# Performance work log

Hardware: AMD Instinct MI355X
Metric: run time of the kernel (lower is better)

The kernel has to match this reference:

```python
import jax, jax.numpy as jnp
import numpy as np

B, T, D, HD = 4, 4096, 1024, 64

def setup_inputs() -> dict:
    key = jax.random.key(0)
    k1, k2, k3, k4 = jax.random.split(key, 4)
    scale = 1.0 / np.sqrt(D)
    return {
        "x": jax.random.normal(k1, (B, T, D), dtype=jnp.float32),
        "Wq": jax.random.normal(k2, (HD, D), dtype=jnp.float32) * scale,
        "Wk": jax.random.normal(k3, (HD, D), dtype=jnp.float32) * scale,
        "Wv": jax.random.normal(k4, (HD, D), dtype=jnp.float32) * scale,
    }

def reference(x, Wq, Wk, Wv):
    # x: [B,T,D]; W*: [head_dim, D] (torch Linear weight layout)
    Q = jnp.einsum('btd,hd->bth', x, Wq)  # [B,T,HD]
    K = jnp.einsum('btd,hd->bth', x, Wk)
    V = jnp.einsum('btd,hd->bth', x, Wv)
    hd = Q.shape[-1]
    scores = jnp.einsum('bqh,bkh->bqk', Q, K) * (hd ** -0.5)  # [B,T,T]
    t = scores.shape[1]
    causal = jnp.tril(jnp.ones((t, t), dtype=bool))
    scores = jnp.where(causal, scores, -jnp.inf)
    att = jax.nn.softmax(scores, axis=-1)
    return jnp.einsum('bqk,bkh->bqh', att, V)  # [B,T,HD]
```

## Files before the change

kernel.cpp:

```cpp
#include <hip/hip_runtime.h>
#include <stdint.h>

#define B_  4
#define T_  4096
#define D_  1024
#define HD_ 64
#define BT_ 16384

typedef short bf16x8 __attribute__((ext_vector_type(8)));
typedef float f32x4  __attribute__((ext_vector_type(4)));
typedef unsigned short u16;
typedef u16 u16x4 __attribute__((ext_vector_type(4)));

#define M0_ 8.0f

__device__ __forceinline__ u16 f2bf(float f) {
    union { float f; unsigned u; } v; v.f = f;
    unsigned r = (v.u + 0x7FFF + ((v.u >> 16) & 1)) >> 16;
    return (u16)r;
}
__device__ __forceinline__ float bf2f(u16 u) {
    union { unsigned u; float f; } v; v.u = ((unsigned)u) << 16;
    return v.f;
}

__device__ __forceinline__ int slot_base(int qt) {
    int a = qt >> 3, r = qt & 7;
    return (a + 1) * (4 * a + r);
}

__global__ __launch_bounds__(256) void wconv_kernel(
    const float* __restrict__ wq, const float* __restrict__ wk,
    const float* __restrict__ wv, u16* __restrict__ wb)
{
    const int j   = blockIdx.x >> 5;
    const int off = (blockIdx.x & 31) * 2048 + threadIdx.x * 8;
    const float* src = (j == 0) ? wq : ((j == 1) ? wk : wv);
    f32x4 a0 = *(const f32x4*)(src + off);
    f32x4 a1 = *(const f32x4*)(src + off + 4);
    bf16x8 b;
    #pragma unroll
    for (int i = 0; i < 4; ++i) { b[i] = (short)f2bf(a0[i]); b[4 + i] = (short)f2bf(a1[i]); }
    *(bf16x8*)(wb + j * 65536 + off) = b;
}

__global__ __launch_bounds__(256) void qkv_kernel(
    const float* __restrict__ x, const u16* __restrict__ wb,
    u16* __restrict__ qs, u16* __restrict__ kss, u16* __restrict__ vssT)
{
    __shared__ __align__(16) u16 xt[16][72];
    __shared__ __align__(16) u16 wt[192][72];

    const int tid  = threadIdx.x;
    const int lane = tid & 63;
    const int w    = tid >> 6;
    const int quad = lane >> 4;
    const int l16  = lane & 15;
    const int row0 = blockIdx.x * 16;

    const int xrow = tid >> 4;
    const int xcg  = tid & 15;

    f32x4 acc[3];
    #pragma unroll
    for (int g = 0; g < 3; ++g) acc[g] = (f32x4)0.0f;

    f32x4  xr;
    bf16x8 wr[6];
    {
        xr = *(const f32x4*)(x + (size_t)(row0 + xrow) * D_ + xcg * 4);
        #pragma unroll
        for (int i = 0; i < 6; ++i) {
            int chunk = tid + 256 * i;
            wr[i] = *(const bf16x8*)(wb + (size_t)(chunk >> 3) * D_ + (chunk & 7) * 8);
        }
    }

    for (int kc = 0; kc < 16; ++kc) {
        __syncthreads();
        {
            u16x4 px;
            #pragma unroll
            for (int i = 0; i < 4; ++i) px[i] = f2bf(xr[i]);
            *(u16x4*)&xt[xrow][xcg * 4] = px;
            #pragma unroll
            for (int i = 0; i < 6; ++i) {
                int chunk = tid + 256 * i;
                *(bf16x8*)&wt[chunk >> 3][(chunk & 7) * 8] = wr[i];
            }
        }
        __syncthreads();
        if (kc < 15) {
            xr = *(const f32x4*)(x + (size_t)(row0 + xrow) * D_ + (kc + 1) * 64 + xcg * 4);
            #pragma unroll
            for (int i = 0; i < 6; ++i) {
                int chunk = tid + 256 * i;
                wr[i] = *(const bf16x8*)(wb + (size_t)(chunk >> 3) * D_ + (kc + 1) * 64 + (chunk & 7) * 8);
            }
        }
        #pragma unroll
        for (int ks = 0; ks < 2; ++ks) {
            bf16x8 a = *(const bf16x8*)&xt[l16][ks * 32 + quad * 8];
            #pragma unroll
            for (int g = 0; g < 3; ++g) {
                bf16x8 b = *(const bf16x8*)&wt[(w * 3 + g) * 16 + l16][ks * 32 + quad * 8];
                acc[g] = __builtin_amdgcn_mfma_f32_16x16x32_bf16(a, b, acc[g], 0, 0, 0);
            }
        }
    }
    #pragma unroll
    for (int g = 0; g < 3; ++g) {
        const int n = (w * 3 + g) * 16 + l16;
        const int j = n >> 6, h = n & 63;
        const int rbase = row0 + quad * 4;
        if (j == 0) {
            #pragma unroll
            for (int r = 0; r < 4; ++r) qs[(size_t)(rbase + r) * HD_ + h] = f2bf(acc[g][r] * 0.125f);
        } else if (j == 1) {
            #pragma unroll
            for (int r = 0; r < 4; ++r) kss[(size_t)(rbase + r) * HD_ + h] = f2bf(acc[g][r]);
        } else {
            u16x4 v;
            #pragma unroll
            for (int r = 0; r < 4; ++r) v[r] = f2bf(acc[g][r]);
            *(u16x4*)(vssT + (size_t)h * BT_ + rbase) = v;
        }
    }
}

__global__ __launch_bounds__(256) void attn_kernel(
    const u16* __restrict__ qs, const u16* __restrict__ kss,
    const u16* __restrict__ vssT,
    float* __restrict__ pl, u16* __restrict__ pO)
{
    __shared__ __align__(16) u16 kt[64][72];
    __shared__ __align__(16) u16 vt[80][72];
    __shared__ __align__(16) u16 pt[4][16][72];

    const int bi = blockIdx.x;
    const int c  = bi & 7;
    const int qt = (bi >> 3) & 63;
    const int b  = bi >> 9;
    const int kt0 = c * 8;
    if (kt0 > qt) return;
    const int kend = ((kt0 + 7) < qt) ? (kt0 + 7) : qt;

    const int tid  = threadIdx.x;
    const int lane = tid & 63;
    const int w    = tid >> 6;
    const int quad = lane >> 4;
    const int l16  = lane & 15;
    const int qb   = qt * 64;
    const size_t base = (size_t)b * T_;

    for (int idx = tid; idx < 16 * 72; idx += 256) {
        int rr = idx / 72, cc = idx - rr * 72;
        vt[64 + rr][cc] = (rr == 0) ? (u16)0x3F80 : (u16)0;
    }

    bf16x8 qf[2];
    {
        const u16* qp = qs + (base + qb + w * 16 + l16) * HD_ + quad * 8;
        qf[0] = *(const bf16x8*)(qp);
        qf[1] = *(const bf16x8*)(qp + 32);
    }

    f32x4 o_acc[5];
    #pragma unroll
    for (int g = 0; g < 5; ++g) o_acc[g] = (f32x4)0.0f;

    const int lr = tid >> 2, lp = tid & 3;

    bf16x8 kr0, kr1, vr0, vr1;
    {
        const u16* sk = kss + (base + kt0 * 64 + lr) * HD_ + lp * 16;
        kr0 = *(const bf16x8*)(sk);  kr1 = *(const bf16x8*)(sk + 8);
        const u16* sv = vssT + (size_t)lr * BT_ + base + kt0 * 64 + lp * 16;
        vr0 = *(const bf16x8*)(sv);  vr1 = *(const bf16x8*)(sv + 8);
    }

    for (int kti = kt0; kti <= kend; ++kti) {
        __syncthreads();
        *(bf16x8*)&kt[lr][lp * 16]     = kr0;
        *(bf16x8*)&kt[lr][lp * 16 + 8] = kr1;
        *(bf16x8*)&vt[lr][lp * 16]     = vr0;
        *(bf16x8*)&vt[lr][lp * 16 + 8] = vr1;
        __syncthreads();
        if (kti < kend) {
            const u16* sk = kss + (base + (kti + 1) * 64 + lr) * HD_ + lp * 16;
            kr0 = *(const bf16x8*)(sk);  kr1 = *(const bf16x8*)(sk + 8);
            const u16* sv = vssT + (size_t)lr * BT_ + base + (kti + 1) * 64 + lp * 16;
            vr0 = *(const bf16x8*)(sv);  vr1 = *(const bf16x8*)(sv + 8);
        }

        f32x4 s[4];
        #pragma unroll
        for (int g = 0; g < 4; ++g) {
            s[g] = (f32x4)0.0f;
            #pragma unroll
            for (int ks = 0; ks < 2; ++ks) {
                bf16x8 kf = *(const bf16x8*)&kt[g * 16 + l16][ks * 32 + quad * 8];
                s[g] = __builtin_amdgcn_mfma_f32_16x16x32_bf16(qf[ks], kf, s[g], 0, 0, 0);
            }
        }
        if (kti == qt) {
            #pragma unroll
            for (int g = 0; g < 4; ++g) {
                int key = kti * 64 + g * 16 + l16;
                #pragma unroll
                for (int r = 0; r < 4; ++r) {
                    int q = qb + w * 16 + quad * 4 + r;
                    if (key > q) s[g][r] = -1e30f;
                }
            }
        }
        #pragma unroll
        for (int g = 0; g < 4; ++g)
            #pragma unroll
            for (int r = 0; r < 4; ++r)
                pt[w][quad * 4 + r][g * 16 + l16] = f2bf(__expf(s[g][r] - M0_));
        #pragma unroll
        for (int ks = 0; ks < 2; ++ks) {
            bf16x8 pa = *(const bf16x8*)&pt[w][l16][ks * 32 + quad * 8];
            #pragma unroll
            for (int g = 0; g < 5; ++g) {
                bf16x8 vf = *(const bf16x8*)&vt[g * 16 + l16][ks * 32 + quad * 8];
                o_acc[g] = __builtin_amdgcn_mfma_f32_16x16x32_bf16(pa, vf, o_acc[g], 0, 0, 0);
            }
        }
    }

    const int slot = b * 288 + slot_base(qt) + c;
    if (l16 == 0) {
        #pragma unroll
        for (int r = 0; r < 4; ++r)
            pl[slot * 64 + w * 16 + quad * 4 + r] = o_acc[4][r];
    }
    #pragma unroll
    for (int g = 0; g < 4; ++g) {
        #pragma unroll
        for (int r = 0; r < 4; ++r) {
            int row = w * 16 + quad * 4 + r;
            pO[(size_t)slot * 4096 + row * 64 + g * 16 + l16] = f2bf(o_acc[g][r]);
        }
    }
}

__global__ __launch_bounds__(256) void merge_kernel(
    const float* __restrict__ pl, const u16* __restrict__ pO,
    float* __restrict__ out)
{
    const int bi = blockIdx.x;
    const int qt = bi & 63, b = bi >> 6;
    const int nc = (qt >> 3) + 1;
    const int s0 = b * 288 + slot_base(qt);
    const int row = threadIdx.x >> 2;
    const int hg  = (threadIdx.x & 3) * 16;

    float L = 0.0f;
    for (int c2 = 0; c2 < nc; ++c2) L += pl[(s0 + c2) * 64 + row];

    float o[16];
    #pragma unroll
    for (int i = 0; i < 16; ++i) o[i] = 0.0f;
    for (int c2 = 0; c2 < nc; ++c2) {
        const u16* p = pO + (size_t)(s0 + c2) * 4096 + row * 64 + hg;
        bf16x8 v0 = *(const bf16x8*)p;
        bf16x8 v1 = *(const bf16x8*)(p + 8);
        #pragma unroll
        for (int i = 0; i < 8; ++i) {
            o[i]     += bf2f((u16)v0[i]);
            o[8 + i] += bf2f((u16)v1[i]);
        }
    }
    const float inv = 1.0f / L;
    float* op = out + ((size_t)b * T_ + qt * 64 + row) * HD_ + hg;
    #pragma unroll
    for (int j = 0; j < 4; ++j) {
        f32x4 v;
        #pragma unroll
        for (int i = 0; i < 4; ++i) v[i] = o[j * 4 + i] * inv;
        *(f32x4*)(op + j * 4) = v;
    }
}

extern "C" void kernel_launch(void* const* d_in, const int* in_sizes, int n_in,
                              void* d_out, int out_size, void* d_ws, size_t ws_size,
                              hipStream_t stream) {
    const float* x  = (const float*)d_in[0];
    const float* wq = (const float*)d_in[1];
    const float* wk = (const float*)d_in[2];
    const float* wv = (const float*)d_in[3];

    const size_t NE = (size_t)BT_ * HD_;
    char* ws = (char*)d_ws;
    u16* qs   = (u16*)ws;
    u16* kss  = qs  + NE;
    u16* vssT = kss + NE;
    u16* wb   = vssT + NE;
    float* pl = (float*)(wb + 192 * 1024);
    u16* pO   = (u16*)(pl + 1152 * 64);
    float* out = (float*)d_out;

    wconv_kernel<<<dim3(96),   dim3(256), 0, stream>>>(wq, wk, wv, wb);
    qkv_kernel  <<<dim3(1024), dim3(256), 0, stream>>>(x, wb, qs, kss, vssT);
    attn_kernel <<<dim3(2048), dim3(256), 0, stream>>>(qs, kss, vssT, pl, pO);
    merge_kernel<<<dim3(256),  dim3(256), 0, stream>>>(pl, pO, out);
}
```

Before: 167.9 us.

## Drop LDS staging for K/V and weights, give each wave its own query strip

```diff
diff --git a/kernel.cpp b/kernel.cpp
--- a/kernel.cpp
+++ b/kernel.cpp
@@ -22,11 +22,6 @@
 __device__ __forceinline__ float bf2f(u16 u) {
     union { unsigned u; float f; } v; v.u = ((unsigned)u) << 16;
     return v.f;
-}
-
-__device__ __forceinline__ int slot_base(int qt) {
-    int a = qt >> 3, r = qt & 7;
-    return (a + 1) * (4 * a + r);
 }
 
 __global__ __launch_bounds__(256) void wconv_kernel(
@@ -44,12 +39,11 @@
     *(bf16x8*)(wb + j * 65536 + off) = b;
 }
 
-__global__ __launch_bounds__(256) void qkv_kernel(
+__global__ __launch_bounds__(256, 5) void qkv_kernel(
     const float* __restrict__ x, const u16* __restrict__ wb,
     u16* __restrict__ qs, u16* __restrict__ kss, u16* __restrict__ vssT)
 {
-    __shared__ __align__(16) u16 xt[16][72];
-    __shared__ __align__(16) u16 wt[192][72];
+    __shared__ __align__(16) u16 xt[2][16][72];
 
     const int tid  = threadIdx.x;
     const int lane = tid & 63;
@@ -61,52 +55,61 @@
     const int xrow = tid >> 4;
     const int xcg  = tid & 15;
 
+    size_t wrow[3];
+    #pragma unroll
+    for (int g = 0; g < 3; ++g) wrow[g] = (size_t)((w * 3 + g) * 16 + l16) * D_;
+
     f32x4 acc[3];
     #pragma unroll
     for (int g = 0; g < 3; ++g) acc[g] = (f32x4)0.0f;
 
-    f32x4  xr;
-    bf16x8 wr[6];
+    const float* xbase = x + (size_t)(row0 + xrow) * D_ + xcg * 4;
+
+    f32x4 xr = *(const f32x4*)(xbase);
     {
-        xr = *(const f32x4*)(x + (size_t)(row0 + xrow) * D_ + xcg * 4);
-        #pragma unroll
-        for (int i = 0; i < 6; ++i) {
-            int chunk = tid + 256 * i;
-            wr[i] = *(const bf16x8*)(wb + (size_t)(chunk >> 3) * D_ + (chunk & 7) * 8);
-        }
-    }
+        u16x4 px;
+        #pragma unroll
+        for (int i = 0; i < 4; ++i) px[i] = f2bf(xr[i]);
+        *(u16x4*)&xt[0][xrow][xcg * 4] = px;
+    }
+    xr = *(const f32x4*)(xbase + 64);
+
+    bf16x8 wcur[6], wnxt[6];
+    #pragma unroll
+    for (int g = 0; g < 3; ++g)
+        #pragma unroll
+        for (int ks = 0; ks < 2; ++ks)
+            wcur[g * 2 + ks] = *(const bf16x8*)(wb + wrow[g] + ks * 32 + quad * 8);
+
+    __syncthreads();
 
     for (int kc = 0; kc < 16; ++kc) {
+        const int p = kc & 1;
+        if (kc + 1 < 16) {
+            u16x4 px;
+            #pragma unroll
+            for (int i = 0; i < 4; ++i) px[i] = f2bf(xr[i]);
+            *(u16x4*)&xt[p ^ 1][xrow][xcg * 4] = px;
+        }
+        if (kc + 2 < 16)
+            xr = *(const f32x4*)(xbase + (kc + 2) * 64);
+        if (kc + 1 < 16) {
+            #pragma unroll
+            for (int g = 0; g < 3; ++g)
+                #pragma unroll
+                for (int ks = 0; ks < 2; ++ks)
+                    wnxt[g * 2 + ks] = *(const bf16x8*)(wb + wrow[g] + (kc + 1) * 64 + ks * 32 + quad * 8);
+        }
+        bf16x8 a0 = *(const bf16x8*)&xt[p][l16][quad * 8];
+        bf16x8 a1 = *(const bf16x8*)&xt[p][l16][32 + quad * 8];
+        #pragma unroll
+        for (int g = 0; g < 3; ++g) {
+            acc[g] = __builtin_amdgcn_mfma_f32_16x16x32_bf16(a0, wcur[g * 2 + 0], acc[g], 0, 0, 0);
+            acc[g] = __builtin_amdgcn_mfma_f32_16x16x32_bf16(a1, wcur[g * 2 + 1], acc[g], 0, 0, 0);
+        }
+        #pragma unroll
+        for (int i = 0; i < 6; ++i) wcur[i] = wnxt[i];
         __syncthreads();
-        {
-            u16x4 px;
-            #pragma unroll
-            for (int i = 0; i < 4; ++i) px[i] = f2bf(xr[i]);
-            *(u16x4*)&xt[xrow][xcg * 4] = px;
-            #pragma unroll
-            for (int i = 0; i < 6; ++i) {
-                int chunk = tid + 256 * i;
-                *(bf16x8*)&wt[chunk >> 3][(chunk & 7) * 8] = wr[i];
-            }
-        }
-        __syncthreads();
-        if (kc < 15) {
-            xr = *(const f32x4*)(x + (size_t)(row0 + xrow) * D_ + (kc + 1) * 64 + xcg * 4);
-            #pragma unroll
-            for (int i = 0; i < 6; ++i) {
-                int chunk = tid + 256 * i;
-                wr[i] = *(const bf16x8*)(wb + (size_t)(chunk >> 3) * D_ + (kc + 1) * 64 + (chunk & 7) * 8);
-            }
-        }
-        #pragma unroll
-        for (int ks = 0; ks < 2; ++ks) {
-            bf16x8 a = *(const bf16x8*)&xt[l16][ks * 32 + quad * 8];
-            #pragma unroll
-            for (int g = 0; g < 3; ++g) {
-                bf16x8 b = *(const bf16x8*)&wt[(w * 3 + g) * 16 + l16][ks * 32 + quad * 8];
-                acc[g] = __builtin_amdgcn_mfma_f32_16x16x32_bf16(a, b, acc[g], 0, 0, 0);
-            }
-        }
     }
     #pragma unroll
     for (int g = 0; g < 3; ++g) {
@@ -128,89 +131,69 @@
     }
 }
 
-__global__ __launch_bounds__(256) void attn_kernel(
+__global__ __launch_bounds__(256, 4) void attn_kernel(
     const u16* __restrict__ qs, const u16* __restrict__ kss,
     const u16* __restrict__ vssT,
     float* __restrict__ pl, u16* __restrict__ pO)
 {
-    __shared__ __align__(16) u16 kt[64][72];
-    __shared__ __align__(16) u16 vt[80][72];
     __shared__ __align__(16) u16 pt[4][16][72];
-
-    const int bi = blockIdx.x;
-    const int c  = bi & 7;
-    const int qt = (bi >> 3) & 63;
-    const int b  = bi >> 9;
-    const int kt0 = c * 8;
-    if (kt0 > qt) return;
-    const int kend = ((kt0 + 7) < qt) ? (kt0 + 7) : qt;
 
     const int tid  = threadIdx.x;
     const int lane = tid & 63;
     const int w    = tid >> 6;
     const int quad = lane >> 4;
     const int l16  = lane & 15;
-    const int qb   = qt * 64;
+
+    const int j   = blockIdx.x * 4 + w;
+    const int b   = j >> 10;
+    const int rem = j & 1023;
+    const int s   = rem >> 2;
+    const int c   = rem & 3;
+    const int dt  = s >> 2;
+    const int kt0 = c * 16;
+    if (kt0 > dt) return;
+    const int kend = (kt0 + 15 < dt) ? (kt0 + 15) : dt;
+
     const size_t base = (size_t)b * T_;
-
-    for (int idx = tid; idx < 16 * 72; idx += 256) {
-        int rr = idx / 72, cc = idx - rr * 72;
-        vt[64 + rr][cc] = (rr == 0) ? (u16)0x3F80 : (u16)0;
-    }
 
     bf16x8 qf[2];
     {
-        const u16* qp = qs + (base + qb + w * 16 + l16) * HD_ + quad * 8;
+        const u16* qp = qs + (base + s * 16 + l16) * HD_ + quad * 8;
         qf[0] = *(const bf16x8*)(qp);
         qf[1] = *(const bf16x8*)(qp + 32);
     }
+    bf16x8 onesf;
+    {
+        u16 ov = (l16 == 0) ? (u16)0x3F80 : (u16)0;
+        #pragma unroll
+        for (int i = 0; i < 8; ++i) onesf[i] = (short)ov;
+    }
 
     f32x4 o_acc[5];
     #pragma unroll
     for (int g = 0; g < 5; ++g) o_acc[g] = (f32x4)0.0f;
 
-    const int lr = tid >> 2, lp = tid & 3;
-
-    bf16x8 kr0, kr1, vr0, vr1;
-    {
-        const u16* sk = kss + (base + kt0 * 64 + lr) * HD_ + lp * 16;
-        kr0 = *(const bf16x8*)(sk);  kr1 = *(const bf16x8*)(sk + 8);
-        const u16* sv = vssT + (size_t)lr * BT_ + base + kt0 * 64 + lp * 16;
-        vr0 = *(const bf16x8*)(sv);  vr1 = *(const bf16x8*)(sv + 8);
-    }
-
     for (int kti = kt0; kti <= kend; ++kti) {
-        __syncthreads();
-        *(bf16x8*)&kt[lr][lp * 16]     = kr0;
-        *(bf16x8*)&kt[lr][lp * 16 + 8] = kr1;
-        *(bf16x8*)&vt[lr][lp * 16]     = vr0;
-        *(bf16x8*)&vt[lr][lp * 16 + 8] = vr1;
-        __syncthreads();
-        if (kti < kend) {
-            const u16* sk = kss + (base + (kti + 1) * 64 + lr) * HD_ + lp * 16;
-            kr0 = *(const bf16x8*)(sk);  kr1 = *(const bf16x8*)(sk + 8);
-            const u16* sv = vssT + (size_t)lr * BT_ + base + (kti + 1) * 64 + lp * 16;
-            vr0 = *(const bf16x8*)(sv);  vr1 = *(const bf16x8*)(sv + 8);
-        }
-
-        f32x4 s[4];
+        const int kb = kti * 64;
+        f32x4 sv[4];
         #pragma unroll
         for (int g = 0; g < 4; ++g) {
-            s[g] = (f32x4)0.0f;
+            sv[g] = (f32x4)0.0f;
             #pragma unroll
             for (int ks = 0; ks < 2; ++ks) {
-                bf16x8 kf = *(const bf16x8*)&kt[g * 16 + l16][ks * 32 + quad * 8];
-                s[g] = __builtin_amdgcn_mfma_f32_16x16x32_bf16(qf[ks], kf, s[g], 0, 0, 0);
+                bf16x8 kf = *(const bf16x8*)(kss + (base + kb + g * 16 + l16) * HD_ + ks * 32 + quad * 8);
+                sv[g] = __builtin_amdgcn_mfma_f32_16x16x32_bf16(qf[ks], kf, sv[g], 0, 0, 0);
             }
         }
-        if (kti == qt) {
+        if (kti == dt) {
             #pragma unroll
             for (int g = 0; g < 4; ++g) {
-                int key = kti * 64 + g * 16 + l16;
+                int key = kb + g * 16 + l16;
                 #pragma unroll
                 for (int r = 0; r < 4; ++r) {
-                    int q = qb + w * 16 + quad * 4 + r;
-                    if (key > q) s[g][r] = -1e30f;
+                    int q = s * 16 + quad * 4 + r;
+                    if (key > q + 0 * 64) { }
+                    if (key > s * 16 + quad * 4 + r) sv[g][r] = -1e30f;
                 }
             }
         }
@@ -218,31 +201,29 @@
         for (int g = 0; g < 4; ++g)
             #pragma unroll
             for (int r = 0; r < 4; ++r)
-                pt[w][quad * 4 + r][g * 16 + l16] = f2bf(__expf(s[g][r] - M0_));
+                pt[w][quad * 4 + r][g * 16 + l16] = f2bf(__expf(sv[g][r] - M0_));
         #pragma unroll
         for (int ks = 0; ks < 2; ++ks) {
             bf16x8 pa = *(const bf16x8*)&pt[w][l16][ks * 32 + quad * 8];
             #pragma unroll
-            for (int g = 0; g < 5; ++g) {
-                bf16x8 vf = *(const bf16x8*)&vt[g * 16 + l16][ks * 32 + quad * 8];
+            for (int g = 0; g < 4; ++g) {
+                bf16x8 vf = *(const bf16x8*)(vssT + (size_t)(g * 16 + l16) * BT_ + base + kb + ks * 32 + quad * 8);
                 o_acc[g] = __builtin_amdgcn_mfma_f32_16x16x32_bf16(pa, vf, o_acc[g], 0, 0, 0);
             }
-        }
-    }
-
-    const int slot = b * 288 + slot_base(qt) + c;
+            o_acc[4] = __builtin_amdgcn_mfma_f32_16x16x32_bf16(pa, onesf, o_acc[4], 0, 0, 0);
+        }
+    }
+
     if (l16 == 0) {
         #pragma unroll
         for (int r = 0; r < 4; ++r)
-            pl[slot * 64 + w * 16 + quad * 4 + r] = o_acc[4][r];
+            pl[j * 16 + quad * 4 + r] = o_acc[4][r];
     }
     #pragma unroll
     for (int g = 0; g < 4; ++g) {
         #pragma unroll
-        for (int r = 0; r < 4; ++r) {
-            int row = w * 16 + quad * 4 + r;
-            pO[(size_t)slot * 4096 + row * 64 + g * 16 + l16] = f2bf(o_acc[g][r]);
-        }
+        for (int r = 0; r < 4; ++r)
+            pO[(size_t)j * 1024 + (quad * 4 + r) * 64 + g * 16 + l16] = f2bf(o_acc[g][r]);
     }
 }
 
@@ -251,20 +232,22 @@
     float* __restrict__ out)
 {
     const int bi = blockIdx.x;
-    const int qt = bi & 63, b = bi >> 6;
-    const int nc = (qt >> 3) + 1;
-    const int s0 = b * 288 + slot_base(qt);
-    const int row = threadIdx.x >> 2;
-    const int hg  = (threadIdx.x & 3) * 16;
+    const int b  = bi >> 6, sg = bi & 63;
+    const int rowl = threadIdx.x >> 2;
+    const int s    = sg * 4 + (rowl >> 4);
+    const int r16  = rowl & 15;
+    const int hg   = (threadIdx.x & 3) * 16;
+    const int nc   = (s >> 6) + 1;
+    const int slot0 = (b * 256 + s) * 4;
 
     float L = 0.0f;
-    for (int c2 = 0; c2 < nc; ++c2) L += pl[(s0 + c2) * 64 + row];
+    for (int c2 = 0; c2 < nc; ++c2) L += pl[(slot0 + c2) * 16 + r16];
 
     float o[16];
     #pragma unroll
     for (int i = 0; i < 16; ++i) o[i] = 0.0f;
     for (int c2 = 0; c2 < nc; ++c2) {
-        const u16* p = pO + (size_t)(s0 + c2) * 4096 + row * 64 + hg;
+        const u16* p = pO + (size_t)(slot0 + c2) * 1024 + r16 * 64 + hg;
         bf16x8 v0 = *(const bf16x8*)p;
         bf16x8 v1 = *(const bf16x8*)(p + 8);
         #pragma unroll
@@ -274,13 +257,13 @@
         }
     }
     const float inv = 1.0f / L;
-    float* op = out + ((size_t)b * T_ + qt * 64 + row) * HD_ + hg;
-    #pragma unroll
-    for (int j = 0; j < 4; ++j) {
+    float* op = out + ((size_t)b * T_ + s * 16 + r16) * HD_ + hg;
+    #pragma unroll
+    for (int jj = 0; jj < 4; ++jj) {
         f32x4 v;
         #pragma unroll
-        for (int i = 0; i < 4; ++i) v[i] = o[j * 4 + i] * inv;
-        *(f32x4*)(op + j * 4) = v;
+        for (int i = 0; i < 4; ++i) v[i] = o[jj * 4 + i] * inv;
+        *(f32x4*)(op + jj * 4) = v;
     }
 }
 
@@ -299,11 +282,11 @@
     u16* vssT = kss + NE;
     u16* wb   = vssT + NE;
     float* pl = (float*)(wb + 192 * 1024);
-    u16* pO   = (u16*)(pl + 1152 * 64);
+    u16* pO   = (u16*)(pl + 4096 * 16);
     float* out = (float*)d_out;
 
     wconv_kernel<<<dim3(96),   dim3(256), 0, stream>>>(wq, wk, wv, wb);
     qkv_kernel  <<<dim3(1024), dim3(256), 0, stream>>>(x, wb, qs, kss, vssT);
-    attn_kernel <<<dim3(2048), dim3(256), 0, stream>>>(qs, kss, vssT, pl, pO);
+    attn_kernel <<<dim3(1024), dim3(256), 0, stream>>>(qs, kss, vssT, pl, pO);
     merge_kernel<<<dim3(256),  dim3(256), 0, stream>>>(pl, pO, out);
 }
```

Result: slower. 255.5 us (+52.2%).
